# Optimization experiments

Measured on AMD Instinct MI355X. Metric: run time of the kernel, lower is better.

## Reference

```python
import jax, jax.numpy as jnp
import numpy as np

# 'linear' blur taps from the source module
_KERNEL_1D = np.array([1/8, 3/8, 3/8, 1/8], dtype=np.float32)


def setup_inputs() -> dict:
    key = jax.random.key(0)
    B, C, H, W = 8, 256, 256, 256
    x = jax.random.normal(key, (B, C, H, W), dtype=jnp.float32)
    # 2D separable blur kernel: outer product of the 1D taps (registered buffer)
    kernel = jnp.asarray(np.outer(_KERNEL_1D, _KERNEL_1D))  # [4, 4]
    return {"x": x, "kernel": kernel}


def reference(x, kernel):
    # pad = k//2 - 1 = 1, reflect padding (torch 'reflect' == numpy 'reflect')
    pad = kernel.shape[0] // 2 - 1
    xp = jnp.pad(x, ((0, 0), (0, 0), (pad, pad), (pad, pad)), mode="reflect")
    C = x.shape[1]
    # Original builds a C x C weight that is zero off-diagonal; math is exactly a
    # depthwise (per-channel) conv with the same 4x4 blur kernel, stride 2.
    w = jnp.broadcast_to(kernel, (C, 1) + kernel.shape)  # [C, 1, 4, 4]
    out = jax.lax.conv_general_dilated(
        xp, w,
        window_strides=(2, 2),
        padding="VALID",
        dimension_numbers=("NCHW", "OIHW", "NCHW"),
        feature_group_count=C,
    )
    return out
```

## Files before the change

kernel.cpp:

```cpp
#include <hip/hip_runtime.h>


#define K0 0.125f
#define K1 0.375f

__global__ __launch_bounds__(256, 8) void downsample2d_kernel(
    const float* __restrict__ x, float* __restrict__ out)
{
    __shared__ float ldsH[34 * 128];

    const int tid   = threadIdx.x;
    const int strip = blockIdx.x & 7;
    const int plane = blockIdx.x >> 3;
    const int oh0   = strip * 16;
    const int ir0   = 2 * oh0 - 1;

    const float* xp = x + (size_t)plane * (256 * 256);

    const int lane = tid & 63;
    const int wave = tid >> 6;

    #pragma unroll
    for (int i = 0; i < 9; ++i) {
        int r = wave + 4 * i;
        if (r < 34) {
            int gr = ir0 + r;
            gr = (gr < 0) ? 1 : ((gr > 255) ? 254 : gr);
            float4 v = *(const float4*)(xp + gr * 256 + (lane << 2));
            float xm1 = __shfl_up(v.w, 1);
            float xp4 = __shfl_down(v.x, 1);
            if (lane == 0)  xm1 = v.y;
            if (lane == 63) xp4 = v.z;
            float h0 = K0 * xm1 + K1 * v.x + K1 * v.y + K0 * v.z;
            float h1 = K0 * v.y + K1 * v.z + K1 * v.w + K0 * xp4;
            *(float2*)(&ldsH[r * 128 + (lane << 1)]) = make_float2(h0, h1);
        }
    }
    __syncthreads();

    const int ow   = tid & 127;
    const int half = tid >> 7;
    const float* L = ldsH + (half << 4) * 128 + ow;

    float* op = out + (size_t)plane * (128 * 128)
                    + (size_t)(oh0 + (half << 3)) * 128 + ow;

    float h0 = L[0];
    float h1 = L[128];
    #pragma unroll
    for (int l = 0; l < 8; ++l) {
        float h2 = L[(2 * l + 2) * 128];
        float h3 = L[(2 * l + 3) * 128];
        op[l * 128] = K0 * h0 + K1 * h1 + K1 * h2 + K0 * h3;
        h0 = h2;
        h1 = h3;
    }
}

extern "C" void kernel_launch(void* const* d_in, const int* in_sizes, int n_in,
                              void* d_out, int out_size, void* d_ws, size_t ws_size,
                              hipStream_t stream) {
    const float* x = (const float*)d_in[0];
    float* out = (float*)d_out;

    const int planes = 8 * 256;
    const int blocks = planes * 8;
    downsample2d_kernel<<<blocks, 256, 0, stream>>>(x, out);
}
```

Before: 712.4 us.

## Give each wave a full strip and slide vertical taps in registers without LDS

Each wavefront now owns one 16-output-row strip and computes the horizontal blur per input row on the fly, keeping a sliding window of four horizontal results in registers for the vertical pass. This removes the shared-memory staging buffer and the block-wide barrier, and stores outputs as float2. The tradeoff is that row loads become a sequential loop per wave, which may expose more memory latency unless the compiler hoists loads across unrolled iterations.

```diff
diff --git a/kernel.cpp b/kernel.cpp
--- a/kernel.cpp
+++ b/kernel.cpp
@@ -7,53 +7,44 @@
 __global__ __launch_bounds__(256, 8) void downsample2d_kernel(
     const float* __restrict__ x, float* __restrict__ out)
 {
-    __shared__ float ldsH[34 * 128];
-
     const int tid   = threadIdx.x;
-    const int strip = blockIdx.x & 7;
-    const int plane = blockIdx.x >> 3;
-    const int oh0   = strip * 16;
-    const int ir0   = 2 * oh0 - 1;
+    const int lane  = tid & 63;
+    const int gw    = (blockIdx.x << 2) + (tid >> 6);
+    const int strip = gw & 7;
+    const int plane = gw >> 3;
+    const int oh0   = strip << 4;
+    const int ir0   = (oh0 << 1) - 1;
 
     const float* xp = x + (size_t)plane * (256 * 256);
+    float* op = out + (size_t)plane * (128 * 128)
+                    + (size_t)oh0 * 128 + (lane << 1);
 
-    const int lane = tid & 63;
-    const int wave = tid >> 6;
+    const int c4 = lane << 2;
 
-    #pragma unroll
-    for (int i = 0; i < 9; ++i) {
-        int r = wave + 4 * i;
-        if (r < 34) {
-            int gr = ir0 + r;
-            gr = (gr < 0) ? 1 : ((gr > 255) ? 254 : gr);
-            float4 v = *(const float4*)(xp + gr * 256 + (lane << 2));
-            float xm1 = __shfl_up(v.w, 1);
-            float xp4 = __shfl_down(v.x, 1);
-            if (lane == 0)  xm1 = v.y;
-            if (lane == 63) xp4 = v.z;
-            float h0 = K0 * xm1 + K1 * v.x + K1 * v.y + K0 * v.z;
-            float h1 = K0 * v.y + K1 * v.z + K1 * v.w + K0 * xp4;
-            *(float2*)(&ldsH[r * 128 + (lane << 1)]) = make_float2(h0, h1);
-        }
-    }
-    __syncthreads();
+    auto loadH = [&](int r) -> float2 {
+        int gr = ir0 + r;
+        gr = (gr < 0) ? 1 : ((gr > 255) ? 254 : gr);
+        float4 v = *(const float4*)(xp + (gr << 8) + c4);
+        float xm1 = __shfl_up(v.w, 1);
+        float xp4 = __shfl_down(v.x, 1);
+        if (lane == 0)  xm1 = v.y;
+        if (lane == 63) xp4 = v.z;
+        return make_float2(K0 * xm1 + K1 * v.x + K1 * v.y + K0 * v.z,
+                           K0 * v.y + K1 * v.z + K1 * v.w + K0 * xp4);
+    };
 
-    const int ow   = tid & 127;
-    const int half = tid >> 7;
-    const float* L = ldsH + (half << 4) * 128 + ow;
-
-    float* op = out + (size_t)plane * (128 * 128)
-                    + (size_t)(oh0 + (half << 3)) * 128 + ow;
-
-    float h0 = L[0];
-    float h1 = L[128];
-    #pragma unroll
-    for (int l = 0; l < 8; ++l) {
-        float h2 = L[(2 * l + 2) * 128];
-        float h3 = L[(2 * l + 3) * 128];
-        op[l * 128] = K0 * h0 + K1 * h1 + K1 * h2 + K0 * h3;
-        h0 = h2;
-        h1 = h3;
+    float2 hA = loadH(0);
+    float2 hB = loadH(1);
+    #pragma unroll 4
+    for (int l = 0; l < 16; ++l) {
+        float2 hC = loadH(2 * l + 2);
+        float2 hD = loadH(2 * l + 3);
+        float2 o;
+        o.x = K0 * hA.x + K1 * hB.x + K1 * hC.x + K0 * hD.x;
+        o.y = K0 * hA.y + K1 * hB.y + K1 * hC.y + K0 * hD.y;
+        *(float2*)(op + l * 128) = o;
+        hA = hC;
+        hB = hD;
     }
 }
 
@@ -64,6 +55,7 @@
     float* out = (float*)d_out;
 
     const int planes = 8 * 256;
-    const int blocks = planes * 8;
+    const int waves  = planes * 8;
+    const int blocks = waves / 4;
     downsample2d_kernel<<<blocks, 256, 0, stream>>>(x, out);
 }
```

Result: no change. 712.4 us (+0.0%).
